# Performance work log

Hardware: AMD Instinct MI355X
Metric: run time of the kernel (lower is better)

## Reference

```python
import jax, jax.numpy as jnp
import numpy as np

DIM = 512
HEADS = 8
DIM_HEAD = DIM * 2 // HEADS  # 128
EPS = 1e-5


def layer_norm(t, g, b):
    mu = jnp.mean(t, axis=-1, keepdims=True)
    var = jnp.var(t, axis=-1, keepdims=True)
    return (t - mu) * jax.lax.rsqrt(var + EPS) * g + b


def rope(q, k):
    # q, k: [b, h, n, d]; standard rotary with half-split rotate_half
    n, d = q.shape[-2], q.shape[-1]
    inv_freq = 1.0 / (10000.0 ** (jnp.arange(0, d, 2, dtype=jnp.float32) / d))
    freqs = jnp.arange(n, dtype=jnp.float32)[:, None] * inv_freq[None, :]  # [n, d/2]
    emb = jnp.concatenate([freqs, freqs], axis=-1)  # [n, d]
    cos, sin = jnp.cos(emb), jnp.sin(emb)

    def rot_half(t):
        t1, t2 = t[..., : d // 2], t[..., d // 2 :]
        return jnp.concatenate([-t2, t1], axis=-1)

    q = q * cos + rot_half(q) * sin
    k = k * cos + rot_half(k) * sin
    return q, k


def setup_inputs() -> dict:
    key = jax.random.key(0)
    ks = jax.random.split(key, 4)
    b, n = 4, 1024
    x = jax.random.normal(ks[0], (b, n, DIM), dtype=jnp.float32)
    a = jax.random.normal(ks[1], (b, n, DIM), dtype=jnp.float32)
    scale = 1.0 / np.sqrt(DIM)
    Wqkv_x = jax.random.normal(ks[2], (DIM, 3 * DIM), dtype=jnp.float32) * scale
    Wqkv_a = jax.random.normal(ks[3], (DIM, 3 * DIM), dtype=jnp.float32) * scale
    ones = jnp.ones((DIM,), jnp.float32)
    zeros = jnp.zeros((DIM,), jnp.float32)
    return {
        "x": x, "a": a, "Wqkv_x": Wqkv_x, "Wqkv_a": Wqkv_a,
        "g_qx": ones, "b_qx": zeros, "g_kx": ones, "b_kx": zeros,
        "g_qa": ones, "b_qa": zeros, "g_ka": ones, "b_ka": zeros,
    }


def reference(x, a, Wqkv_x, Wqkv_a, g_qx, b_qx, g_kx, b_kx, g_qa, b_qa, g_ka, b_ka):
    b, n, _ = x.shape

    qkv_x = x @ Wqkv_x  # [b, n, 3*dim]
    q_x, k_x, v_x = jnp.split(qkv_x, 3, axis=-1)
    q_x = layer_norm(q_x, g_qx, b_qx)
    k_x = layer_norm(k_x, g_kx, b_kx)

    qkv_a = a @ Wqkv_a
    q_a, k_a, v_a = jnp.split(qkv_a, 3, axis=-1)
    q_a = layer_norm(q_a, g_qa, b_qa)
    k_a = layer_norm(k_a, g_ka, b_ka)

    q = jnp.concatenate([q_x, q_a], axis=-1)  # [b, n, 2*dim]
    k = jnp.concatenate([k_x, k_a], axis=-1)
    v = jnp.concatenate([v_x, v_a], axis=-1)

    def to_heads(t):
        return t.reshape(b, n, HEADS, DIM_HEAD).transpose(0, 2, 1, 3)  # [b,h,n,d]

    q, k, v = to_heads(q), to_heads(k), to_heads(v)
    q, k = rope(q, k)

    scale = 1.0 / np.sqrt(DIM_HEAD)
    scores = jnp.einsum("bhqd,bhkd->bhqk", q, k) * scale
    attn = jax.nn.softmax(scores, axis=-1)
    out = jnp.einsum("bhqk,bhkd->bhqd", attn, v)  # [b,h,n,d]
    out = out.transpose(0, 2, 1, 3).reshape(b, n, HEADS * DIM_HEAD)  # [b,n,2*dim]
    return out
```

## Files before the change

kernel.cpp:

```cpp
#include <hip/hip_runtime.h>
#include <math.h>

typedef __attribute__((ext_vector_type(8))) short bf16x8;
typedef __attribute__((ext_vector_type(4))) short bf16x4;
typedef __attribute__((ext_vector_type(4))) float f32x4;
typedef __attribute__((ext_vector_type(16))) float f32x16;

#define BB    4
#define SEQ   1024
#define DIMV  512
#define TD    1536
#define NH    8
#define DH    128
#define MROWS (BB*SEQ)

__device__ inline unsigned short f2bf(float x){
    union { float f; unsigned u; } v; v.f = x;
    unsigned r = v.u + 0x7FFF + ((v.u >> 16) & 1);
    return (unsigned short)(r >> 16);
}
__device__ inline float bf2f(unsigned short h){
    union { unsigned u; float f; } v; v.u = ((unsigned)h) << 16; return v.f;
}

__device__ inline void glds16(const void* g, void* l){
    __builtin_amdgcn_global_load_lds(
        (const __attribute__((address_space(1))) unsigned int*)g,
        (__attribute__((address_space(3))) unsigned int*)l,
        16, 0, 0);
}

__global__ __launch_bounds__(256) void prep_a(
    const float* __restrict__ X, const float* __restrict__ A,
    unsigned short* __restrict__ Ab)
{
    const int m   = blockIdx.x*256 + threadIdx.x;
    const int pg  = blockIdx.y;
    const int mat = blockIdx.z;
    const float* In = mat ? A : X;
    const float* src = In + (size_t)m*DIMV + pg*8;
    float4 v0 = *(const float4*)src;
    float4 v1 = *(const float4*)(src+4);
    float v[8] = {v0.x,v0.y,v0.z,v0.w,v1.x,v1.y,v1.z,v1.w};
    bf16x8 h;
    #pragma unroll
    for (int j=0;j<8;++j) h[j] = (short)f2bf(v[j]);
    const size_t o = ((size_t)(mat*64 + pg)*4096 + m)*8;
    *(bf16x8*)(Ab+o) = h;
}

__global__ __launch_bounds__(256) void prep_b(
    const float* __restrict__ Wx, const float* __restrict__ Wa,
    unsigned short* __restrict__ Bhi, unsigned short* __restrict__ Blo,
    float2* __restrict__ tab)
{
    if (blockIdx.x == 6){
        const int i = (blockIdx.z*64 + blockIdx.y)*256 + threadIdx.x;
        #pragma unroll
        for (int k=0;k<2;++k){
            const int idx = i + k*32768;
            const int n = idx >> 6, dd = idx & 63;
            const float inv = expf((float)dd * (1.f/64.f) * -9.210340371976184f);
            const float ang = (float)n * inv;
            float sn, cs;
            sincosf(ang, &sn, &cs);
            tab[idx] = make_float2(cs, sn);
        }
        return;
    }
    const int n   = blockIdx.x*256 + threadIdx.x;
    const int pg  = blockIdx.y;
    const int mat = blockIdx.z;
    const float* W = mat ? Wa : Wx;
    bf16x8 h, l;
    #pragma unroll
    for (int j=0;j<8;++j){
        float v = W[(size_t)(pg*8 + j)*TD + n];
        unsigned short hb = f2bf(v);
        h[j] = (short)hb;
        l[j] = (short)f2bf(v - bf2f(hb));
    }
    const size_t o = ((size_t)(mat*64 + pg)*1536 + n)*8;
    *(bf16x8*)(Bhi+o) = h;
    *(bf16x8*)(Blo+o) = l;
}

__global__ __launch_bounds__(256,3) void qkv_mfma(
    const unsigned short* __restrict__ Ab,
    const unsigned short* __restrict__ Bhi, const unsigned short* __restrict__ Blo,
    unsigned short* __restrict__ wsqb, unsigned short* __restrict__ wskb,
    unsigned short* __restrict__ Vf)
{
    __shared__ __align__(16) unsigned short sA [8192];
    __shared__ __align__(16) unsigned short sBh[8192];
    __shared__ __align__(16) unsigned short sBl[8192];

    const int mat = blockIdx.z;
    const int bm  = blockIdx.x * 128;
    const int bn  = blockIdx.y * 128;
    const bool vblk = (bn >= 1024);
    const int tid = threadIdx.x;
    const int w   = tid >> 6, l = tid & 63;
    const int wr  = w >> 1,  wc = w & 1;
    const int lg  = l >> 4,  ln = l & 15;

    f32x4 acc[4][4];
    #pragma unroll
    for (int i=0;i<4;++i)
        #pragma unroll
        for (int j=0;j<4;++j){ acc[i][j][0]=0.f; acc[i][j][1]=0.f; acc[i][j][2]=0.f; acc[i][j][3]=0.f; }

    const int g0 = tid >> 7, r0 = tid & 127;
    const size_t ASTEP = (size_t)8*4096*8;
    const size_t BSTEP = (size_t)8*1536*8;
    const unsigned short* aP = Ab  + ((size_t)(mat*64 + g0)*4096 + bm + r0)*8;
    const unsigned short* bPh = Bhi + ((size_t)(mat*64 + g0)*1536 + bn + r0)*8;
    const unsigned short* bPl = Blo + ((size_t)(mat*64 + g0)*1536 + bn + r0)*8;
    const size_t AC = (size_t)2*4096*8;
    const size_t BC = (size_t)2*1536*8;

    if (vblk){
        for (int p=0; p<8; ++p){
            #pragma unroll
            for (int c=0;c<4;++c){
                glds16(aP  + c*AC, sA  + (c*256+tid)*8);
                glds16(bPh + c*BC, sBh + (c*256+tid)*8);
                glds16(bPl + c*BC, sBl + (c*256+tid)*8);
            }
            aP += ASTEP; bPh += BSTEP; bPl += BSTEP;
            __syncthreads();

            #pragma unroll
            for (int kk=0;kk<2;++kk){
                bf16x8 av[4], bh[4], bl[4];
                #pragma unroll
                for (int mi=0; mi<4; ++mi){
                    const int off = ((kk*4+lg)*128 + wr*64 + mi*16 + ln)*8;
                    av[mi] = *(const bf16x8*)(sA + off);
                }
                #pragma unroll
                for (int ni=0; ni<4; ++ni){
                    const int off = ((kk*4+lg)*128 + wc*64 + ni*16 + ln)*8;
                    bh[ni] = *(const bf16x8*)(sBh + off);
                    bl[ni] = *(const bf16x8*)(sBl + off);
                }
                #pragma unroll
                for (int mi=0; mi<4; ++mi)
                    #pragma unroll
                    for (int ni=0; ni<4; ++ni){
                        acc[mi][ni] = __builtin_amdgcn_mfma_f32_16x16x32_bf16(av[mi], bh[ni], acc[mi][ni], 0,0,0);
                        acc[mi][ni] = __builtin_amdgcn_mfma_f32_16x16x32_bf16(av[mi], bl[ni], acc[mi][ni], 0,0,0);
                    }
            }
            __syncthreads();
        }
    } else {
        for (int p=0; p<8; ++p){
            #pragma unroll
            for (int c=0;c<4;++c){
                glds16(aP  + c*AC, sA  + (c*256+tid)*8);
                glds16(bPh + c*BC, sBh + (c*256+tid)*8);
            }
            aP += ASTEP; bPh += BSTEP;
            __syncthreads();

            #pragma unroll
            for (int kk=0;kk<2;++kk){
                bf16x8 av[4], bh[4];
                #pragma unroll
                for (int mi=0; mi<4; ++mi){
                    const int off = ((kk*4+lg)*128 + wr*64 + mi*16 + ln)*8;
                    av[mi] = *(const bf16x8*)(sA + off);
                }
                #pragma unroll
                for (int ni=0; ni<4; ++ni){
                    const int off = ((kk*4+lg)*128 + wc*64 + ni*16 + ln)*8;
                    bh[ni] = *(const bf16x8*)(sBh + off);
                }
                #pragma unroll
                for (int mi=0; mi<4; ++mi)
                    #pragma unroll
                    for (int ni=0; ni<4; ++ni)
                        acc[mi][ni] = __builtin_amdgcn_mfma_f32_16x16x32_bf16(av[mi], bh[ni], acc[mi][ni], 0,0,0);
            }
            __syncthreads();
        }
    }

    const int b_ = bm >> 10;
    const int n0base = (bm & 1023) + wr*64;
    const int colB = bn + wc*64;
    if (!vblk){
        unsigned short* base = (colB < 512) ? wsqb : wskb;
        #pragma unroll
        for (int ni=0; ni<4; ++ni){
            const int col = colB + ni*16 + ln;
            const int h = mat*4 + ((col >> 7) & 3);
            const int d = col & 127;
            #pragma unroll
            for (int mi=0; mi<4; ++mi){
                const int n0 = n0base + mi*16 + lg*4;
                unsigned short* dst = base + ((size_t)(b_*NH + h)*SEQ + n0)*DH + d;
                #pragma unroll
                for (int r=0;r<4;++r) dst[r*DH] = f2bf(acc[mi][ni][r]);
            }
        }
    } else {
        #pragma unroll
        for (int ni=0; ni<4; ++ni){
            const int col = colB + ni*16 + ln;
            const int h  = mat*4 + ((col >> 7) & 3);
            const int d  = col & 127;
            const int dt = d >> 5;
            const int lane = (d & 31) + 32*(lg >> 1);
            const int bh = b_*NH + h;
            #pragma unroll
            for (int mi=0; mi<4; ++mi){
                const int kt = (n0base + mi*16) >> 5;
                const int kc = mi & 1;
                unsigned short* dst = Vf +
                    ((((size_t)(bh*32 + kt)*2 + kc)*4 + dt)*64 + lane)*8 + (lg&1)*4;
                bf16x4 pk;
                #pragma unroll
                for (int r=0;r<4;++r) pk[r] = (short)f2bf(acc[mi][ni][r]);
                *(bf16x4*)dst = pk;
            }
        }
    }
}

__global__ __launch_bounds__(256) void ln_rope(
    const unsigned short* __restrict__ wsqb, const unsigned short* __restrict__ wskb,
    unsigned short* __restrict__ Qb, unsigned short* __restrict__ Kb,
    const float2* __restrict__ tab,
    const float* __restrict__ g_qx, const float* __restrict__ b_qx,
    const float* __restrict__ g_kx, const float* __restrict__ b_kx,
    const float* __restrict__ g_qa, const float* __restrict__ b_qa,
    const float* __restrict__ g_ka, const float* __restrict__ b_ka)
{
    const int w0   = threadIdx.x >> 6;
    const int lane = threadIdx.x & 63;
    const int inst = blockIdx.x*4 + w0;
    const int which = inst & 3;
    const int r = inst >> 2;
    const int b_ = r >> 10, n_ = r & 1023;

    const unsigned short* buf = (which & 1) ? wskb : wsqb;
    unsigned short* ob = (which & 1) ? Kb : Qb;
    const int h0 = (which >> 1) ? 4 : 0;
    const float* g; const float* bb;
    if (which==0){ g=g_qx; bb=b_qx; }
    else if (which==1){ g=g_kx; bb=b_kx; }
    else if (which==2){ g=g_qa; bb=b_qa; }
    else { g=g_ka; bb=b_ka; }

    const int hc = lane >> 4;
    const int h  = h0 + hc;
    const int d0 = (lane & 15) * 8;
    const size_t idx = ((size_t)(b_*NH + h)*SEQ + n_)*DH + d0;

    bf16x8 vin = *(const bf16x8*)(buf + idx);
    float v[8];
    float s1 = 0.f, s2 = 0.f;
    #pragma unroll
    for (int j=0;j<8;++j){
        v[j] = bf2f((unsigned short)vin[j]);
        s1 += v[j]; s2 += v[j]*v[j];
    }
    #pragma unroll
    for (int off=1; off<64; off<<=1){
        s1 += __shfl_xor(s1, off);
        s2 += __shfl_xor(s2, off);
    }
    const float mu = s1 * (1.f/512.f);
    const float var = s2 * (1.f/512.f) - mu*mu;
    const float rs = rsqrtf(var + 1e-5f);

    const int e = lane*8;
    float4 gv0 = *(const float4*)(g + e);
    float4 gv1 = *(const float4*)(g + e + 4);
    float4 bv0 = *(const float4*)(bb + e);
    float4 bv1 = *(const float4*)(bb + e + 4);
    const float gg[8]  = {gv0.x,gv0.y,gv0.z,gv0.w,gv1.x,gv1.y,gv1.z,gv1.w};
    const float bbv[8] = {bv0.x,bv0.y,bv0.z,bv0.w,bv1.x,bv1.y,bv1.z,bv1.w};

    float xn[8];
    #pragma unroll
    for (int j=0;j<8;++j) xn[j] = (v[j]-mu)*rs*gg[j] + bbv[j];

    float pr[8];
    #pragma unroll
    for (int j=0;j<8;++j) pr[j] = __shfl_xor(xn[j], 8);

    const bool firsthalf = (lane & 8) == 0;
    const float2* tp = tab + (n_ << 6) + (lane & 7)*8;
    const float qs = 0.08838834764831845f * 1.4426950408889634f;
    bf16x8 outv;
    #pragma unroll
    for (int j=0;j<8;++j){
        const float2 cs = tp[j];
        const float rot = firsthalf ? -pr[j] : pr[j];
        float val = xn[j]*cs.x + rot*cs.y;
        if (!(which & 1)) val *= qs;
        outv[j] = (short)f2bf(val);
    }
    *(bf16x8*)(ob + idx) = outv;
}

__global__ __launch_bounds__(256,2) void attn_mfma(
    const unsigned short* __restrict__ Qb, const unsigned short* __restrict__ Kb,
    const unsigned short* __restrict__ Vf, float* __restrict__ out)
{
    __shared__ __align__(16) unsigned short SMEM[32768];

    const int nblk = blockIdx.x;
    const int jj  = nblk >> 3;
    const int bh  = (nblk & 7)*4 + (jj >> 4);
    const int q0  = (jj & 15) * 64;

    const int tid = threadIdx.x;
    const int w   = tid >> 6;
    const int qg  = w >> 1;
    const int ks  = w & 1;
    const int l   = tid & 63;
    const int lq  = l & 31;
    const int h   = l >> 5;
    const size_t hoff = (size_t)bh * SEQ * DH;

    bf16x8 qf[8];
    {
        const unsigned short* qp = Qb + hoff + (size_t)(q0 + qg*32 + lq)*DH + h*8;
        #pragma unroll
        for (int dc=0;dc<8;++dc) qf[dc] = *(const bf16x8*)(qp + dc*16);
    }

    f32x16 o[4];
    #pragma unroll
    for (int dt=0;dt<4;++dt)
        #pragma unroll
        for (int i=0;i<16;++i) o[dt][i] = 0.f;
    float mrun = -INFINITY, lrun = 0.f;

    const unsigned short* kg0 = Kb + hoff;
    const unsigned short* vt0 = Vf + (size_t)bh*32*4096 + l*8;

    #define STAGE_K(bb, grp) { \
        unsigned short* base_ = SMEM + (bb)*16384; \
        const unsigned short* ks_ = kg0 + (size_t)(4*(grp))*4096; \
        _Pragma("unroll") \
        for (int t_=0;t_<4;++t_) \
            _Pragma("unroll") \
            for (int i_=0;i_<2;++i_){ \
                int f_ = tid + i_*256; int r_ = f_>>4, s_ = f_&15; \
                glds16(ks_ + t_*4096 + r_*128 + ((s_ ^ (r_&7))*8), base_ + t_*4096 + f_*8); \
            } }

    #define LOADV(VF_, tile) { \
        const unsigned short* vb_ = vt0 + (size_t)(tile)*4096; \
        _Pragma("unroll") \
        for (int kc_=0;kc_<2;++kc_) \
            _Pragma("unroll") \
            for (int dt_=0;dt_<4;++dt_) \
                VF_[kc_][dt_] = *(const bf16x8*)(vb_ + (kc_*4+dt_)*512); }

    #define SUB(slot, VF_) { \
        const unsigned short* kb = SMEM + cur*16384 + (slot)*4096 + lq*128; \
        f32x16 s; \
        _Pragma("unroll") \
        for (int i=0;i<16;++i) s[i] = 0.f; \
        _Pragma("unroll") \
        for (int dc=0;dc<8;++dc){ \
            bf16x8 kf = *(const bf16x8*)(kb + (((dc*2+h) ^ (lq&7))*8)); \
            s = __builtin_amdgcn_mfma_f32_32x32x16_bf16(kf, qf[dc], s, 0,0,0); \
        } \
        float mx = fmaxf(s[0], s[1]); \
        _Pragma("unroll") \
        for (int i=2;i<16;++i) mx = fmaxf(mx, s[i]); \
        mx = fmaxf(mx, __shfl_xor(mx, 32)); \
        if (__any(mx > mrun + 8.f)){ \
            const float mn = fmaxf(mrun, mx); \
            const float al = __builtin_amdgcn_exp2f(mrun - mn); \
            mrun = mn; lrun *= al; \
            _Pragma("unroll") \
            for (int dt=0;dt<4;++dt) \
                _Pragma("unroll") \
                for (int i=0;i<16;++i) o[dt][i] *= al; \
        } \
        float su = 0.f; \
        _Pragma("unroll") \
        for (int i=0;i<16;++i){ s[i] = __builtin_amdgcn_exp2f(s[i]-mrun); su += s[i]; } \
        su += __shfl_xor(su, 32); \
        lrun += su; \
        bf16x8 pf[2]; \
        _Pragma("unroll") \
        for (int kc=0; kc<2; ++kc){ \
            const int b8 = kc*8; \
            unsigned A, Bq, Cq, Dq; \
            asm("v_cvt_pk_bf16_f32 %0, %1, %2" : "=v"(A)  : "v"(s[b8+0]), "v"(s[b8+1])); \
            asm("v_cvt_pk_bf16_f32 %0, %1, %2" : "=v"(Bq) : "v"(s[b8+2]), "v"(s[b8+3])); \
            asm("v_cvt_pk_bf16_f32 %0, %1, %2" : "=v"(Cq) : "v"(s[b8+4]), "v"(s[b8+5])); \
            asm("v_cvt_pk_bf16_f32 %0, %1, %2" : "=v"(Dq) : "v"(s[b8+6]), "v"(s[b8+7])); \
            asm("v_permlane32_swap_b32 %0, %1" : "+v"(A),  "+v"(Cq)); \
            asm("v_permlane32_swap_b32 %0, %1" : "+v"(Bq), "+v"(Dq)); \
            union { unsigned u[4]; bf16x8 v; } pk; \
            pk.u[0] = A; pk.u[1] = Bq; pk.u[2] = Cq; pk.u[3] = Dq; \
            pf[kc] = pk.v; \
        } \
        _Pragma("unroll") \
        for (int kc=0;kc<2;++kc) \
            _Pragma("unroll") \
            for (int dt=0;dt<4;++dt) \
                o[dt] = __builtin_amdgcn_mfma_f32_32x32x16_bf16(VF_[kc][dt], pf[kc], o[dt], 0,0,0); }

    bf16x8 vf0[2][4], vf1[2][4];

    STAGE_K(0, 0);
    __syncthreads();

    int cur = 0;
    for (int ii=0; ii<8; ++ii){
        LOADV(vf0, 4*ii + ks);
        LOADV(vf1, 4*ii + 2 + ks);
        if (ii < 7) STAGE_K(cur^1, ii+1);
        SUB(ks,     vf0);
        SUB(2 + ks, vf1);
        __syncthreads();
        cur ^= 1;
    }
    #undef SUB
    #undef STAGE_K
    #undef LOADV

    float* Lm = (float*)SMEM;
    float* Ll = Lm + 128;
    Lm[(qg*2+ks)*32 + lq] = mrun;
    Ll[(qg*2+ks)*32 + lq] = lrun;
    __syncthreads();
    const float mo  = Lm[(qg*2+(ks^1))*32 + lq];
    const float lo_ = Ll[(qg*2+(ks^1))*32 + lq];
    const float mf = fmaxf(mrun, mo);
    const float a  = __builtin_amdgcn_exp2f(mrun - mf);
    const float ao = __builtin_amdgcn_exp2f(mo - mf);
    const float lf = lrun*a + lo_*ao;
    float* Ob = (float*)SMEM + 512 + qg*4160;
    if (ks == 1){
        #pragma unroll
        for (int dt=0;dt<4;++dt)
            #pragma unroll
            for (int r=0;r<16;++r){
                const int d = dt*32 + (r&3) + 8*(r>>2) + 4*h;
                Ob[lq*129 + d] = o[dt][r]*a;
            }
    }
    __syncthreads();
    if (ks == 0){
        const float inv = 1.0f/lf;
        #pragma unroll
        for (int dt=0;dt<4;++dt)
            #pragma unroll
            for (int r=0;r<16;++r){
                const int d = dt*32 + (r&3) + 8*(r>>2) + 4*h;
                const int idx = lq*129 + d;
                Ob[idx] = (o[dt][r]*a + Ob[idx])*inv;
            }
    }
    __syncthreads();
    const int b_ = bh >> 3, h_ = bh & 7;
    const int row = tid >> 2, quarter = tid & 3;
    const float* src = (const float*)SMEM + 512 + (row>>5)*4160 + (row&31)*129 + quarter*32;
    float* dst = out + ((size_t)(b_*SEQ) + q0 + row)*1024 + h_*128 + quarter*32;
    #pragma unroll
    for (int j=0;j<8;++j)
        *(float4*)(dst + j*4) = *(const float4*)(src + j*4);
}

extern "C" void kernel_launch(void* const* d_in, const int* in_sizes, int n_in,
                              void* d_out, int out_size, void* d_ws, size_t ws_size,
                              hipStream_t stream) {
    const float* x    = (const float*)d_in[0];
    const float* a    = (const float*)d_in[1];
    const float* Wx   = (const float*)d_in[2];
    const float* Wa   = (const float*)d_in[3];
    const float* g_qx = (const float*)d_in[4];
    const float* b_qx = (const float*)d_in[5];
    const float* g_kx = (const float*)d_in[6];
    const float* b_kx = (const float*)d_in[7];
    const float* g_qa = (const float*)d_in[8];
    const float* b_qa = (const float*)d_in[9];
    const float* g_ka = (const float*)d_in[10];
    const float* b_ka = (const float*)d_in[11];
    float* out = (float*)d_out;

    const size_t E = (size_t)BB*NH*SEQ*DH;
    unsigned short* wsqb = (unsigned short*)d_ws;
    unsigned short* wskb = wsqb + E;
    unsigned short* Vf   = wskb + E;
    unsigned short* region = Vf + E;
    unsigned short* Ab  = region;
    unsigned short* Qb  = region;
    unsigned short* Kb  = region + E;
    unsigned short* Bhi = region + 2*E;
    unsigned short* Blo = Bhi + (size_t)2*64*1536*8;
    float2* tab = (float2*)(Blo + (size_t)2*64*1536*8);

    prep_a<<<dim3(16, 64, 2), 256, 0, stream>>>(x, a, Ab);
    prep_b<<<dim3(7, 64, 2), 256, 0, stream>>>(Wx, Wa, Bhi, Blo, tab);
    qkv_mfma<<<dim3(32, 12, 2), 256, 0, stream>>>(Ab, Bhi, Blo, wsqb, wskb, Vf);
    ln_rope<<<dim3(4096), 256, 0, stream>>>(wsqb, wskb, Qb, Kb, tab,
        g_qx, b_qx, g_kx, b_kx, g_qa, b_qa, g_ka, b_ka);
    attn_mfma<<<dim3(512), 256, 0, stream>>>(Qb, Kb, Vf, out);
}
```

Measured before the change: 73.91 us.

## Triple-buffer K tiles in attention, add MFMA priority hints, merge prep kernels

The attention kernel moves from a double buffer holding four K tiles per stage to a three-slot ring of two-tile stages. Loads are issued two phases ahead and guarded by an explicit vmcnt wait and raw barriers, and the loop runs 16 times instead of 8. This cuts LDS use and may raise occupancy or overlap. MFMA sections are wrapped in s_setprio to favour matrix issue. The two prep kernels are merged into one launch to save launch overhead. The hand-written waitcnt and barrier ordering risks races if vmcnt accounting is off.

```diff
diff --git a/kernel.cpp b/kernel.cpp
--- a/kernel.cpp
+++ b/kernel.cpp
@@ -30,32 +30,44 @@
         16, 0, 0);
 }
 
-__global__ __launch_bounds__(256) void prep_a(
+__global__ __launch_bounds__(256) void prep_all(
     const float* __restrict__ X, const float* __restrict__ A,
-    unsigned short* __restrict__ Ab)
-{
-    const int m   = blockIdx.x*256 + threadIdx.x;
-    const int pg  = blockIdx.y;
-    const int mat = blockIdx.z;
-    const float* In = mat ? A : X;
-    const float* src = In + (size_t)m*DIMV + pg*8;
-    float4 v0 = *(const float4*)src;
-    float4 v1 = *(const float4*)(src+4);
-    float v[8] = {v0.x,v0.y,v0.z,v0.w,v1.x,v1.y,v1.z,v1.w};
-    bf16x8 h;
-    #pragma unroll
-    for (int j=0;j<8;++j) h[j] = (short)f2bf(v[j]);
-    const size_t o = ((size_t)(mat*64 + pg)*4096 + m)*8;
-    *(bf16x8*)(Ab+o) = h;
-}
-
-__global__ __launch_bounds__(256) void prep_b(
+    unsigned short* __restrict__ Ab,
     const float* __restrict__ Wx, const float* __restrict__ Wa,
     unsigned short* __restrict__ Bhi, unsigned short* __restrict__ Blo,
     float2* __restrict__ tab)
 {
-    if (blockIdx.x == 6){
-        const int i = (blockIdx.z*64 + blockIdx.y)*256 + threadIdx.x;
+    const int bx  = blockIdx.x;
+    const int pg  = blockIdx.y;
+    const int mat = blockIdx.z;
+    if (bx < 16){
+        const int m = bx*256 + threadIdx.x;
+        const float* In = mat ? A : X;
+        const float* src = In + (size_t)m*DIMV + pg*8;
+        float4 v0 = *(const float4*)src;
+        float4 v1 = *(const float4*)(src+4);
+        float v[8] = {v0.x,v0.y,v0.z,v0.w,v1.x,v1.y,v1.z,v1.w};
+        bf16x8 h;
+        #pragma unroll
+        for (int j=0;j<8;++j) h[j] = (short)f2bf(v[j]);
+        const size_t o = ((size_t)(mat*64 + pg)*4096 + m)*8;
+        *(bf16x8*)(Ab+o) = h;
+    } else if (bx < 22){
+        const int n = (bx-16)*256 + threadIdx.x;
+        const float* W = mat ? Wa : Wx;
+        bf16x8 h, l;
+        #pragma unroll
+        for (int j=0;j<8;++j){
+            float v = W[(size_t)(pg*8 + j)*TD + n];
+            unsigned short hb = f2bf(v);
+            h[j] = (short)hb;
+            l[j] = (short)f2bf(v - bf2f(hb));
+        }
+        const size_t o = ((size_t)(mat*64 + pg)*1536 + n)*8;
+        *(bf16x8*)(Bhi+o) = h;
+        *(bf16x8*)(Blo+o) = l;
+    } else {
+        const int i = (mat*64 + pg)*256 + threadIdx.x;
         #pragma unroll
         for (int k=0;k<2;++k){
             const int idx = i + k*32768;
@@ -66,23 +78,7 @@
             sincosf(ang, &sn, &cs);
             tab[idx] = make_float2(cs, sn);
         }
-        return;
-    }
-    const int n   = blockIdx.x*256 + threadIdx.x;
-    const int pg  = blockIdx.y;
-    const int mat = blockIdx.z;
-    const float* W = mat ? Wa : Wx;
-    bf16x8 h, l;
-    #pragma unroll
-    for (int j=0;j<8;++j){
-        float v = W[(size_t)(pg*8 + j)*TD + n];
-        unsigned short hb = f2bf(v);
-        h[j] = (short)hb;
-        l[j] = (short)f2bf(v - bf2f(hb));
-    }
-    const size_t o = ((size_t)(mat*64 + pg)*1536 + n)*8;
-    *(bf16x8*)(Bhi+o) = h;
-    *(bf16x8*)(Blo+o) = l;
+    }
 }
 
 __global__ __launch_bounds__(256,3) void qkv_mfma(
@@ -311,7 +307,7 @@
     const unsigned short* __restrict__ Qb, const unsigned short* __restrict__ Kb,
     const unsigned short* __restrict__ Vf, float* __restrict__ out)
 {
-    __shared__ __align__(16) unsigned short SMEM[32768];
+    __shared__ __align__(16) unsigned short SMEM[24576];
 
     const int nblk = blockIdx.x;
     const int jj  = nblk >> 3;
@@ -344,15 +340,15 @@
     const unsigned short* kg0 = Kb + hoff;
     const unsigned short* vt0 = Vf + (size_t)bh*32*4096 + l*8;
 
-    #define STAGE_K(bb, grp) { \
-        unsigned short* base_ = SMEM + (bb)*16384; \
-        const unsigned short* ks_ = kg0 + (size_t)(4*(grp))*4096; \
-        _Pragma("unroll") \
-        for (int t_=0;t_<4;++t_) \
+    #define STAGE_K(bb, ph) { \
+        unsigned short* kd_ = SMEM + (bb)*8192; \
+        const unsigned short* ksrc_ = kg0 + (size_t)(2*(ph))*4096; \
+        _Pragma("unroll") \
+        for (int t_=0;t_<2;++t_) \
             _Pragma("unroll") \
             for (int i_=0;i_<2;++i_){ \
                 int f_ = tid + i_*256; int r_ = f_>>4, s_ = f_&15; \
-                glds16(ks_ + t_*4096 + r_*128 + ((s_ ^ (r_&7))*8), base_ + t_*4096 + f_*8); \
+                glds16(ksrc_ + t_*4096 + r_*128 + ((s_ ^ (r_&7))*8), kd_ + t_*4096 + f_*8); \
             } }
 
     #define LOADV(VF_, tile) { \
@@ -363,16 +359,18 @@
             for (int dt_=0;dt_<4;++dt_) \
                 VF_[kc_][dt_] = *(const bf16x8*)(vb_ + (kc_*4+dt_)*512); }
 
-    #define SUB(slot, VF_) { \
-        const unsigned short* kb = SMEM + cur*16384 + (slot)*4096 + lq*128; \
+    #define SUB(slotbase, VF_) { \
+        const unsigned short* kb = SMEM + (slotbase)*8192 + ks*4096 + lq*128; \
         f32x16 s; \
         _Pragma("unroll") \
         for (int i=0;i<16;++i) s[i] = 0.f; \
+        __builtin_amdgcn_s_setprio(1); \
         _Pragma("unroll") \
         for (int dc=0;dc<8;++dc){ \
             bf16x8 kf = *(const bf16x8*)(kb + (((dc*2+h) ^ (lq&7))*8)); \
             s = __builtin_amdgcn_mfma_f32_32x32x16_bf16(kf, qf[dc], s, 0,0,0); \
         } \
+        __builtin_amdgcn_s_setprio(0); \
         float mx = fmaxf(s[0], s[1]); \
         _Pragma("unroll") \
         for (int i=2;i<16;++i) mx = fmaxf(mx, s[i]); \
@@ -395,42 +393,53 @@
         _Pragma("unroll") \
         for (int kc=0; kc<2; ++kc){ \
             const int b8 = kc*8; \
-            unsigned A, Bq, Cq, Dq; \
-            asm("v_cvt_pk_bf16_f32 %0, %1, %2" : "=v"(A)  : "v"(s[b8+0]), "v"(s[b8+1])); \
+            unsigned Aq, Bq, Cq, Dq; \
+            asm("v_cvt_pk_bf16_f32 %0, %1, %2" : "=v"(Aq) : "v"(s[b8+0]), "v"(s[b8+1])); \
             asm("v_cvt_pk_bf16_f32 %0, %1, %2" : "=v"(Bq) : "v"(s[b8+2]), "v"(s[b8+3])); \
             asm("v_cvt_pk_bf16_f32 %0, %1, %2" : "=v"(Cq) : "v"(s[b8+4]), "v"(s[b8+5])); \
             asm("v_cvt_pk_bf16_f32 %0, %1, %2" : "=v"(Dq) : "v"(s[b8+6]), "v"(s[b8+7])); \
-            asm("v_permlane32_swap_b32 %0, %1" : "+v"(A),  "+v"(Cq)); \
+            asm("v_permlane32_swap_b32 %0, %1" : "+v"(Aq), "+v"(Cq)); \
             asm("v_permlane32_swap_b32 %0, %1" : "+v"(Bq), "+v"(Dq)); \
             union { unsigned u[4]; bf16x8 v; } pk; \
-            pk.u[0] = A; pk.u[1] = Bq; pk.u[2] = Cq; pk.u[3] = Dq; \
+            pk.u[0] = Aq; pk.u[1] = Bq; pk.u[2] = Cq; pk.u[3] = Dq; \
             pf[kc] = pk.v; \
         } \
+        __builtin_amdgcn_s_setprio(1); \
         _Pragma("unroll") \
         for (int kc=0;kc<2;++kc) \
             _Pragma("unroll") \
             for (int dt=0;dt<4;++dt) \
-                o[dt] = __builtin_amdgcn_mfma_f32_32x32x16_bf16(VF_[kc][dt], pf[kc], o[dt], 0,0,0); }
-
-    bf16x8 vf0[2][4], vf1[2][4];
+                o[dt] = __builtin_amdgcn_mfma_f32_32x32x16_bf16(VF_[kc][dt], pf[kc], o[dt], 0,0,0); \
+        __builtin_amdgcn_s_setprio(0); }
+
+    bf16x8 vf[2][4];
 
     STAGE_K(0, 0);
-    __syncthreads();
-
-    int cur = 0;
-    for (int ii=0; ii<8; ++ii){
-        LOADV(vf0, 4*ii + ks);
-        LOADV(vf1, 4*ii + 2 + ks);
-        if (ii < 7) STAGE_K(cur^1, ii+1);
-        SUB(ks,     vf0);
-        SUB(2 + ks, vf1);
-        __syncthreads();
-        cur ^= 1;
+    STAGE_K(1, 1);
+    asm volatile("s_waitcnt vmcnt(4)" ::: "memory");
+    __builtin_amdgcn_s_barrier();
+    __builtin_amdgcn_sched_barrier(0);
+
+    int rd = 0;
+    for (int i=0; i<16; ++i){
+        LOADV(vf, 2*i + ks);
+        __builtin_amdgcn_sched_barrier(0);
+        if (i < 14){
+            int wr = rd + 2; if (wr >= 3) wr -= 3;
+            STAGE_K(wr, i+2);
+        }
+        __builtin_amdgcn_sched_barrier(0);
+        SUB(rd, vf);
+        __builtin_amdgcn_sched_barrier(0);
+        if (i < 15) __builtin_amdgcn_s_barrier();
+        __builtin_amdgcn_sched_barrier(0);
+        rd = (rd + 1 == 3) ? 0 : rd + 1;
     }
     #undef SUB
     #undef STAGE_K
     #undef LOADV
 
+    __syncthreads();
     float* Lm = (float*)SMEM;
     float* Ll = Lm + 128;
     Lm[(qg*2+ks)*32 + lq] = mrun;
@@ -503,8 +512,7 @@
     unsigned short* Blo = Bhi + (size_t)2*64*1536*8;
     float2* tab = (float2*)(Blo + (size_t)2*64*1536*8);
 
-    prep_a<<<dim3(16, 64, 2), 256, 0, stream>>>(x, a, Ab);
-    prep_b<<<dim3(7, 64, 2), 256, 0, stream>>>(Wx, Wa, Bhi, Blo, tab);
+    prep_all<<<dim3(23, 64, 2), 256, 0, stream>>>(x, a, Ab, Wx, Wa, Bhi, Blo, tab);
     qkv_mfma<<<dim3(32, 12, 2), 256, 0, stream>>>(Ab, Bhi, Blo, wsqb, wskb, Vf);
     ln_rope<<<dim3(4096), 256, 0, stream>>>(wsqb, wskb, Qb, Kb, tab,
         g_qx, b_qx, g_kx, b_kx, g_qa, b_qa, g_ka, b_ka);
```

After: 80.21 us. 1.09x slower.
